# Performance work log

Measured on AMD Instinct MI355X. Metric: run time of the kernel, lower is better.

Reference implementation:

```python
import jax, jax.numpy as jnp
import numpy as np

Ng, Np, T, B = 2048, 512, 100, 256


def setup_inputs() -> dict:
    key = jax.random.key(0)
    ks = jax.random.split(key, 16)
    s = lambda fan_in: 1.0 / np.sqrt(fan_in)
    return {
        "v": jax.random.normal(ks[0], (B, T, 2), jnp.float32),
        "p0": jax.random.uniform(ks[1], (B, Np), jnp.float32),
        "enc1_W": jax.random.normal(ks[2], (Np, Ng), jnp.float32) * s(Np),
        "enc1_b": jnp.zeros((Ng,), jnp.float32),
        "enc2_W": jax.random.normal(ks[3], (Np, Ng), jnp.float32) * s(Np),
        "enc2_b": jnp.zeros((Ng,), jnp.float32),
        "M_W": jax.random.normal(ks[4], (2, Ng), jnp.float32) * s(2),
        "M_b": jnp.zeros((Ng,), jnp.float32),
        "lstm_W": jax.random.normal(ks[5], (Ng, 4 * Ng), jnp.float32) * s(Ng),
        "lstm_U": jax.random.normal(ks[6], (Ng, 4 * Ng), jnp.float32) * s(Ng),
        "lstm_b": jnp.zeros((4 * Ng,), jnp.float32),
        "dense_W": jax.random.normal(ks[7], (Ng, Ng), jnp.float32) * s(Ng),
        "dense_b": jnp.zeros((Ng,), jnp.float32),
        "dec_W": jax.random.normal(ks[8], (Ng, Np), jnp.float32) * s(Ng),
        "dec_b": jnp.zeros((Np,), jnp.float32),
    }


def reference(v, p0, enc1_W, enc1_b, enc2_W, enc2_b, M_W, M_b,
              lstm_W, lstm_U, lstm_b, dense_W, dense_b, dec_W, dec_b):
    # initial LSTM state from place-cell code: (h0, c0)
    h0 = p0 @ enc1_W + enc1_b                      # [B, Ng]
    c0 = p0 @ enc2_W + enc2_b                      # [B, Ng]
    Mv = v @ M_W + M_b                             # [B, T, Ng]
    # precompute input-to-gate projections for all timesteps
    x_gates = Mv @ lstm_W + lstm_b                 # [B, T, 4*Ng]

    def step(carry, xt):
        h, c = carry
        z = xt + h @ lstm_U                        # [B, 4*Ng]
        i, f, g, o = jnp.split(z, 4, axis=-1)      # Keras gate order i,f,c,o
        i = jax.nn.sigmoid(i)
        f = jax.nn.sigmoid(f)
        g = jax.nn.relu(g)                         # activation='relu'
        o = jax.nn.sigmoid(o)
        c = f * c + i * g
        h = o * jax.nn.relu(c)
        return (h, c), h

    xs = jnp.swapaxes(x_gates, 0, 1)               # [T, B, 4*Ng]
    _, hs = jax.lax.scan(step, (h0, c0), xs)       # hs: [T, B, Ng]
    rnn = jnp.swapaxes(hs, 0, 1)                   # [B, T, Ng]
    g_cells = jax.nn.relu(rnn @ dense_W + dense_b) # [B, T, Ng]
    place_preds = g_cells @ dec_W + dec_b          # [B, T, Np]
    return place_preds
```

## Files before the change

kernel.cpp:

```cpp
#include <hip/hip_runtime.h>
#include <stdint.h>

#define DI __device__ __forceinline__

typedef short s16x8 __attribute__((ext_vector_type(8)));
typedef float f32x4 __attribute__((ext_vector_type(4)));

#define NG   2048
#define NP   512
#define TT   100
#define BB   256
#define N4   8192
#define MR   25600
#define NBLK 256

DI unsigned short f32_to_bf16(float f) {
  union { float f; uint32_t u; } x; x.f = f;
  uint32_t r = x.u + 0x7fffu + ((x.u >> 16) & 1u);
  return (unsigned short)(r >> 16);
}

DI void async16(const void* g, void* l) {
  __builtin_amdgcn_global_load_lds((const __attribute__((address_space(1))) void*)g,
                                   (__attribute__((address_space(3))) void*)l,
                                   16, 0, 0);
}
DI void async4(const void* g, void* l) {
  __builtin_amdgcn_global_load_lds((const __attribute__((address_space(1))) void*)g,
                                   (__attribute__((address_space(3))) void*)l,
                                   4, 0, 0);
}

DI f32x4 mfma16(s16x8 a, s16x8 b, f32x4 c) {
  return __builtin_amdgcn_mfma_f32_16x16x32_bf16(a, b, c, 0, 0, 0);
}

__global__ __launch_bounds__(256) void k_zero(unsigned* p) {
  if (threadIdx.x < 160) p[threadIdx.x] = 0u;
}

DI void grid_barrier2(unsigned* bar, int xcd, int t) {
  asm volatile("s_waitcnt vmcnt(0)" ::: "memory");
  __syncthreads();
  if (threadIdx.x == 0) {
    unsigned a = __hip_atomic_fetch_add(bar + xcd * 16, 1u,
                                        __ATOMIC_RELAXED, __HIP_MEMORY_SCOPE_AGENT);
    if (a + 1u == 32u * (unsigned)(t + 1)) {
      unsigned g2 = __hip_atomic_fetch_add(bar + 128, 1u,
                                           __ATOMIC_RELAXED, __HIP_MEMORY_SCOPE_AGENT);
      if (g2 + 1u == 8u * (unsigned)(t + 1))
        __hip_atomic_store(bar + 144, (unsigned)(t + 1),
                           __ATOMIC_RELAXED, __HIP_MEMORY_SCOPE_AGENT);
    }
    while (__hip_atomic_load(bar + 144, __ATOMIC_RELAXED,
                             __HIP_MEMORY_SCOPE_AGENT) < (unsigned)(t + 1))
      __builtin_amdgcn_s_sleep(8);
  }
  __syncthreads();
}

template <int BM>
DI void gemm_core_p(const unsigned short* __restrict__ A, int lda, int m0,
                    const unsigned short* __restrict__ Bt, int ldb, int n0, int K,
                    unsigned short* sA, unsigned short* sB, f32x4* acc) {
  constexpr int FM = BM / 32;
  const int tid  = threadIdx.x;
  const int wave = tid >> 6;
  const int lane = tid & 63;
  const int quad = lane >> 4;
  const int lr   = lane & 15;
  const int wm   = wave >> 2;
  const int wn   = wave & 3;
  const int lr8  = lane >> 3;
  const int lc8  = lane & 7;
  const int scol = (lc8 ^ lr8) << 3;

  const int nkt = K >> 6;
  int buf = 0;

  auto stage = [&](int bsel, int k0) {
    unsigned short* dA = sA + bsel * (BM * 64);
    unsigned short* dB = sB + bsel * (128 * 64);
#pragma unroll
    for (int c = 0; c < BM / 64; ++c) {
      int rbase = wave * (BM / 8) + c * 8;
      const unsigned short* g = A + (size_t)(m0 + rbase + lr8) * lda + (k0 + scol);
      async16(g, dA + rbase * 64);
    }
#pragma unroll
    for (int c = 0; c < 2; ++c) {
      int rbase = wave * 16 + c * 8;
      const unsigned short* g = Bt + (size_t)(n0 + rbase + lr8) * ldb + (k0 + scol);
      async16(g, dB + rbase * 64);
    }
  };

  stage(0, 0);
  __syncthreads();
  for (int kt = 0; kt < nkt; ++kt) {
    if (kt + 1 < nkt) stage(buf ^ 1, (kt + 1) << 6);
    const char* cA = (const char*)(sA + buf * (BM * 64));
    const char* cB = (const char*)(sB + buf * (128 * 64));
#pragma unroll
    for (int ks = 0; ks < 2; ++ks) {
      s16x8 af[FM], bfr[2];
#pragma unroll
      for (int fm = 0; fm < FM; ++fm) {
        int row = wm * (BM / 2) + fm * 16 + lr;
        int off = row * 128 + ((ks * 64 + quad * 16) ^ ((row & 7) << 4));
        af[fm] = *(const s16x8*)(cA + off);
      }
#pragma unroll
      for (int fn = 0; fn < 2; ++fn) {
        int col = wn * 32 + fn * 16 + lr;
        int off = col * 128 + ((ks * 64 + quad * 16) ^ ((col & 7) << 4));
        bfr[fn] = *(const s16x8*)(cB + off);
      }
#pragma unroll
      for (int fm = 0; fm < FM; ++fm)
#pragma unroll
        for (int fn = 0; fn < 2; ++fn)
          acc[fm * 2 + fn] = mfma16(af[fm], bfr[fn], acc[fm * 2 + fn]);
    }
    __syncthreads();
    buf ^= 1;
  }
}

template <int MODE>
__global__ __launch_bounds__(256) void k_transpose_bf16(
    const float* __restrict__ src, unsigned short* __restrict__ dst,
    int R, int C, int noff) {
  __shared__ unsigned short tile[64][65];
  int tr0 = blockIdx.x * 64;
  int tc0 = blockIdx.y * 64;
  int tid = threadIdx.x;
#pragma unroll
  for (int i = 0; i < 16; ++i) {
    int idx = tid + i * 256;
    int r = idx >> 6, c = idx & 63;
    tile[r][c] = f32_to_bf16(src[(size_t)(tr0 + r) * C + (tc0 + c)]);
  }
  __syncthreads();
#pragma unroll
  for (int i = 0; i < 16; ++i) {
    int idx = tid + i * 256;
    int cc = idx >> 6, r = idx & 63;
    int c = tc0 + cc;
    int n = (MODE == 0) ? (c + noff)
                        : ((((c & 2047) >> 4) << 6) | (((c >> 11) & 3) << 4) | (c & 15));
    dst[(size_t)n * R + (tr0 + r)] = tile[r][cc];
  }
}

__global__ __launch_bounds__(256) void k_cvt(const float* __restrict__ src,
                                             unsigned short* __restrict__ dst, int n) {
  int i = blockIdx.x * 256 + threadIdx.x;
  if (i < n) dst[i] = f32_to_bf16(src[i]);
}

__global__ __launch_bounds__(256) void k_prep_xw_part(
    const float* __restrict__ lstm_W, const float* __restrict__ M_W,
    const float* __restrict__ M_b, float* __restrict__ part) {
  int c = blockIdx.x * 256 + threadIdx.x;
  int kc = blockIdx.y;
  int k0 = kc * 128;
  float a0 = 0.f, a1 = 0.f, ab = 0.f;
  for (int k = k0; k < k0 + 128; ++k) {
    float w = lstm_W[(size_t)k * N4 + c];
    a0 += M_W[k] * w;
    a1 += M_W[NG + k] * w;
    ab += M_b[k] * w;
  }
  float* p = part + (size_t)kc * 3 * N4;
  p[c] = a0; p[N4 + c] = a1; p[2 * N4 + c] = ab;
}

__global__ __launch_bounds__(256) void k_prep_xw_reduce(
    const float* __restrict__ part, const float* __restrict__ lstm_b,
    float* __restrict__ W2r, float* __restrict__ b2r) {
  int c = blockIdx.x * 256 + threadIdx.x;
  float a0 = 0.f, a1 = 0.f, ab = 0.f;
  for (int kc = 0; kc < 16; ++kc) {
    const float* p = part + (size_t)kc * 3 * N4;
    a0 += p[c]; a1 += p[N4 + c]; ab += p[2 * N4 + c];
  }
  int n = (((c & 2047) >> 4) << 6) | (((c >> 11) & 3) << 4) | (c & 15);
  W2r[n] = a0; W2r[N4 + n] = a1; b2r[n] = ab + lstm_b[c];
}

__global__ __launch_bounds__(512) void k_enc(
    const unsigned short* __restrict__ p0b, const unsigned short* __restrict__ encWt,
    const float* __restrict__ enc1_b, const float* __restrict__ enc2_b,
    unsigned short* __restrict__ hbf, float* __restrict__ cfp) {
  __shared__ __align__(16) unsigned short sA[2 * 64 * 64];
  __shared__ __align__(16) unsigned short sB[2 * 128 * 64];
  int m0 = blockIdx.x * 64, n0 = blockIdx.y * 128;
  const f32x4 vzero = {0.f, 0.f, 0.f, 0.f};
  f32x4 acc[4];
#pragma unroll
  for (int i = 0; i < 4; ++i) acc[i] = vzero;
  gemm_core_p<64>(p0b, NP, m0, encWt, NP, n0, NP, sA, sB, acc);

  const int tid = threadIdx.x, wave = tid >> 6, lane = tid & 63;
  const int quad = lane >> 4, lr = lane & 15, wm = wave >> 2, wn = wave & 3;
#pragma unroll
  for (int fm = 0; fm < 2; ++fm)
#pragma unroll
    for (int fn = 0; fn < 2; ++fn)
#pragma unroll
      for (int reg = 0; reg < 4; ++reg) {
        int grow = m0 + wm * 32 + fm * 16 + quad * 4 + reg;
        int gcol = n0 + wn * 32 + fn * 16 + lr;
        float val = acc[fm * 2 + fn][reg];
        if (gcol < NG)
          hbf[(size_t)grow * NG + gcol] = f32_to_bf16(val + enc1_b[gcol]);
        else
          cfp[(size_t)grow * NG + (gcol - NG)] = val + enc2_b[gcol - NG];
      }
}

__global__ __launch_bounds__(256) void k_steps(
    const unsigned short* __restrict__ Ut,
    const float* __restrict__ vv, const float* __restrict__ W2r,
    const float* __restrict__ b2r, const float* __restrict__ cfp,
    const unsigned short* __restrict__ hb0,
    unsigned short* __restrict__ hs, unsigned* __restrict__ bar) {
  __shared__ __align__(16) char smem[127488];

  const int bid = blockIdx.x;
  const int xcd = bid & 7, sb = bid >> 3;
  const int mt = sb >> 3, nsub = sb & 7;
  const int nt = xcd * 8 + nsub;
  const int m0 = mt * 64, n0 = nt * 128;
  const int tid = threadIdx.x;
  const int wave = tid >> 6, lane = tid & 63;
  const int quad = lane >> 4, lr = lane & 15;
  const int wm = wave >> 1, wn = wave & 1;
  const int lr8 = lane >> 3, lc8 = lane & 7;
  const int scol = (lc8 ^ lr8) << 3;

  float w2x[4], w2y[4], bz[4];
#pragma unroll
  for (int g = 0; g < 4; ++g) {
    const int idx = n0 + wn * 64 + g * 16 + lr;
    w2x[g] = W2r[idx]; w2y[g] = W2r[N4 + idx]; bz[g] = b2r[idx];
    asm volatile("" : "+v"(w2x[g])); asm volatile("" : "+v"(w2y[g]));
    asm volatile("" : "+v"(bz[g]));
  }
  const int cellg = nt * 32 + wn * 16 + lr;
  float cst[2][4];
#pragma unroll
  for (int fm = 0; fm < 2; ++fm)
#pragma unroll
    for (int reg = 0; reg < 4; ++reg) {
      const int r = wm * 32 + fm * 16 + quad * 4 + reg;
      cst[fm][reg] = cfp[(size_t)(m0 + r) * NG + cellg];
      asm volatile("" : "+v"(cst[fm][reg]));
    }

  auto stageA = [&](int slot, int kt, const unsigned short* hin) {
#pragma unroll
    for (int c = 0; c < 2; ++c) {
      const int rb = wave * 16 + c * 8;
      const unsigned short* g = hin + (size_t)(m0 + rb + lr8) * NG + ((kt << 6) + scol);
      async16(g, smem + slot * 8192 + rb * 128);
    }
  };
  auto stageB = [&](int slot, int k) {
#pragma unroll
    for (int c = 0; c < 4; ++c) {
      const int rb = wave * 32 + c * 8;
      const unsigned short* g = Ut + (size_t)(n0 + rb + lr8) * NG + (k + scol);
      async16(g, smem + 40960 + slot * 16384 + rb * 128);
    }
  };
  auto stageV = [&](int t) {
    const float* gx = vv + ((size_t)(m0 + lane) * TT + t) * 2;
    async4(gx, smem + 122880);
    async4(gx + 1, smem + 123136);
  };

  f32x4 acc[8];
  auto computeS = [&](int slot) {
    const char* cA = smem + slot * 8192;
    const char* cB = smem + 40960 + slot * 16384;
#pragma unroll
    for (int ks = 0; ks < 2; ++ks) {
      s16x8 af[2], bfr[4];
#pragma unroll
      for (int fm = 0; fm < 2; ++fm) {
        const int row = wm * 32 + fm * 16 + lr;
        af[fm] = *(const s16x8*)(cA + row * 128 + ((ks * 64 + quad * 16) ^ ((row & 7) << 4)));
      }
#pragma unroll
      for (int fn = 0; fn < 4; ++fn) {
        const int col = wn * 64 + fn * 16 + lr;
        bfr[fn] = *(const s16x8*)(cB + col * 128 + ((ks * 64 + quad * 16) ^ ((col & 7) << 4)));
      }
#pragma unroll
      for (int fm = 0; fm < 2; ++fm)
#pragma unroll
        for (int fn = 0; fn < 4; ++fn)
          acc[fm * 4 + fn] = mfma16(af[fm], bfr[fn], acc[fm * 4 + fn]);
    }
  };

#define INC5(x) x = ((x) == 4) ? 0 : ((x) + 1)
#define PHASE(W)  asm volatile("s_waitcnt vmcnt(" #W ")\n\ts_barrier" ::: "memory"); \
                  computeS(cs); INC5(cs);

  asm volatile("s_waitcnt vmcnt(0)" ::: "memory");
  int cs = 0;
  stageB(0, 0); stageB(1, 64); stageB(2, 128);

  for (int t = 0; t < TT; ++t) {
    const unsigned short* hin = t ? hs + (size_t)(t - 1) * BB * NG : hb0;
    {
      int s1 = cs; stageA(s1, 0, hin); INC5(s1);
      stageA(s1, 1, hin); INC5(s1);
      stageA(s1, 2, hin);
    }
    stageV(t);
    const f32x4 vzero = {0.f, 0.f, 0.f, 0.f};
#pragma unroll
    for (int i = 0; i < 8; ++i) acc[i] = vzero;

    int ss = cs; INC5(ss); INC5(ss); INC5(ss);
    stageB(ss, 3 << 6); stageA(ss, 3, hin); INC5(ss);
    PHASE(12)
    stageB(ss, 4 << 6); stageA(ss, 4, hin); INC5(ss);
    PHASE(16)
    stageB(ss, 5 << 6); stageA(ss, 5, hin); INC5(ss);
    PHASE(20)
    for (int p = 3; p <= 28; ++p) {
      stageB(ss, (p + 3) << 6); stageA(ss, p + 3, hin); INC5(ss);
      PHASE(18)
    }
    stageB(ss, 0); INC5(ss);
    PHASE(16)
    stageB(ss, 64); INC5(ss);
    PHASE(14)
    stageB(ss, 128); INC5(ss);
    PHASE(12)

    const float* vx = (const float*)(smem + 122880);
    const float* vy = (const float*)(smem + 123136);
    unsigned short* htmp = (unsigned short*)(smem + 123392);
#pragma unroll
    for (int fm = 0; fm < 2; ++fm)
#pragma unroll
      for (int reg = 0; reg < 4; ++reg) {
        const int r = wm * 32 + fm * 16 + quad * 4 + reg;
        const float ax = vx[r], ay = vy[r];
        float zi = acc[fm * 4 + 0][reg] + ax * w2x[0] + ay * w2y[0] + bz[0];
        float zf = acc[fm * 4 + 1][reg] + ax * w2x[1] + ay * w2y[1] + bz[1];
        float zg = acc[fm * 4 + 2][reg] + ax * w2x[2] + ay * w2y[2] + bz[2];
        float zo = acc[fm * 4 + 3][reg] + ax * w2x[3] + ay * w2y[3] + bz[3];
        float i_ = 1.f / (1.f + __expf(-zi));
        float f_ = 1.f / (1.f + __expf(-zf));
        float g_ = fmaxf(zg, 0.f);
        float o_ = 1.f / (1.f + __expf(-zo));
        float cn = f_ * cst[fm][reg] + i_ * g_;
        cst[fm][reg] = cn;
        htmp[r * 32 + wn * 16 + lr] = f32_to_bf16(o_ * fmaxf(cn, 0.f));
      }
    __syncthreads();
    const unsigned* hw = (const unsigned*)htmp;
#pragma unroll
    for (int p = 0; p < 4; ++p) {
      const int q = tid + p * 256;
      const int r = q >> 4, cq = q & 15;
      unsigned* hp = (unsigned*)(hs + ((size_t)t * BB + m0 + r) * NG) + (nt * 16 + cq);
      __hip_atomic_store(hp, hw[q], __ATOMIC_RELAXED, __HIP_MEMORY_SCOPE_AGENT);
    }
    if (t + 1 < TT) grid_barrier2(bar, xcd, t);
  }
#undef PHASE
#undef INC5
}

__global__ __launch_bounds__(512) void k_dense(
    const unsigned short* __restrict__ hs, const unsigned short* __restrict__ dWt,
    const float* __restrict__ dense_b, unsigned short* __restrict__ gc) {
  __shared__ __align__(16) unsigned short sA[2 * 128 * 64];
  __shared__ __align__(16) unsigned short sB[2 * 128 * 64];
  int bid = blockIdx.x;
  int mt = bid >> 4;
  int r4 = bid & 15;
  int nt = ((r4 & 7) << 1) | (r4 >> 3);
  int m0 = mt * 128, n0 = nt * 128;
  const f32x4 vzero = {0.f, 0.f, 0.f, 0.f};
  f32x4 acc[8];
#pragma unroll
  for (int i = 0; i < 8; ++i) acc[i] = vzero;
  gemm_core_p<128>(hs, NG, m0, dWt, NG, n0, NG, sA, sB, acc);

  const int tid = threadIdx.x, wave = tid >> 6, lane = tid & 63;
  const int quad = lane >> 4, lr = lane & 15, wm = wave >> 2, wn = wave & 3;
#pragma unroll
  for (int fm = 0; fm < 4; ++fm)
#pragma unroll
    for (int fn = 0; fn < 2; ++fn)
#pragma unroll
      for (int reg = 0; reg < 4; ++reg) {
        int grow = m0 + wm * 64 + fm * 16 + quad * 4 + reg;
        int gcol = n0 + wn * 32 + fn * 16 + lr;
        float val = fmaxf(acc[fm * 2 + fn][reg] + dense_b[gcol], 0.f);
        gc[(size_t)grow * NG + gcol] = f32_to_bf16(val);
      }
}

__global__ __launch_bounds__(512) void k_dec(
    const unsigned short* __restrict__ gc, const unsigned short* __restrict__ decWt,
    const float* __restrict__ dec_b, float* __restrict__ out) {
  __shared__ __align__(16) unsigned short sA[2 * 128 * 64];
  __shared__ __align__(16) unsigned short sB[2 * 128 * 64];
  int m0 = blockIdx.x * 128, n0 = blockIdx.y * 128;
  const f32x4 vzero = {0.f, 0.f, 0.f, 0.f};
  f32x4 acc[8];
#pragma unroll
  for (int i = 0; i < 8; ++i) acc[i] = vzero;
  gemm_core_p<128>(gc, NG, m0, decWt, NG, n0, NG, sA, sB, acc);

  const int tid = threadIdx.x, wave = tid >> 6, lane = tid & 63;
  const int quad = lane >> 4, lr = lane & 15, wm = wave >> 2, wn = wave & 3;
#pragma unroll
  for (int fm = 0; fm < 4; ++fm)
#pragma unroll
    for (int fn = 0; fn < 2; ++fn)
#pragma unroll
      for (int reg = 0; reg < 4; ++reg) {
        int grow = m0 + wm * 64 + fm * 16 + quad * 4 + reg;
        int gcol = n0 + wn * 32 + fn * 16 + lr;
        int tt = grow >> 8, b = grow & 255;
        out[((size_t)b * TT + tt) * NP + gcol] = acc[fm * 2 + fn][reg] + dec_b[gcol];
      }
}

extern "C" void kernel_launch(void* const* d_in, const int* in_sizes, int n_in,
                              void* d_out, int out_size, void* d_ws, size_t ws_size,
                              hipStream_t stream) {
  (void)in_sizes; (void)n_in; (void)out_size; (void)ws_size;
  const float* v       = (const float*)d_in[0];
  const float* p0      = (const float*)d_in[1];
  const float* enc1_W  = (const float*)d_in[2];
  const float* enc1_b  = (const float*)d_in[3];
  const float* enc2_W  = (const float*)d_in[4];
  const float* enc2_b  = (const float*)d_in[5];
  const float* M_W     = (const float*)d_in[6];
  const float* M_b     = (const float*)d_in[7];
  const float* lstm_W  = (const float*)d_in[8];
  const float* lstm_U  = (const float*)d_in[9];
  const float* lstm_b  = (const float*)d_in[10];
  const float* dense_W = (const float*)d_in[11];
  const float* dense_b = (const float*)d_in[12];
  const float* dec_W   = (const float*)d_in[13];
  const float* dec_b   = (const float*)d_in[14];
  float* out = (float*)d_out;

  char* ws = (char*)d_ws;
  size_t off = 0;
  auto alloc = [&](size_t bytes) {
    char* p = ws + off;
    off += (bytes + 255) & ~(size_t)255;
    return p;
  };
  unsigned short* Ut    = (unsigned short*)alloc((size_t)N4 * NG * 2);
  unsigned short* dWt   = (unsigned short*)alloc((size_t)NG * NG * 2);
  unsigned short* decWt = (unsigned short*)alloc((size_t)NP * NG * 2);
  unsigned short* encWt = (unsigned short*)alloc((size_t)2 * NG * NP * 2);
  unsigned short* p0b   = (unsigned short*)alloc((size_t)BB * NP * 2);
  float* W2r  = (float*)alloc((size_t)2 * N4 * 4);
  float* b2r  = (float*)alloc((size_t)N4 * 4);
  float* part = (float*)alloc((size_t)16 * 3 * N4 * 4);
  float* cfp  = (float*)alloc((size_t)BB * NG * 4);
  unsigned short* hb0 = (unsigned short*)alloc((size_t)BB * NG * 2);
  unsigned short* hs  = (unsigned short*)alloc((size_t)MR * NG * 2);
  unsigned short* gc  = (unsigned short*)alloc((size_t)MR * NG * 2);
  unsigned* bar = (unsigned*)alloc(1024);

  dim3 blk(256), blk5(512);
  k_zero<<<dim3(1), blk, 0, stream>>>(bar);
  k_transpose_bf16<1><<<dim3(32, 128), blk, 0, stream>>>(lstm_U, Ut, NG, N4, 0);
  k_transpose_bf16<0><<<dim3(32, 32), blk, 0, stream>>>(dense_W, dWt, NG, NG, 0);
  k_transpose_bf16<0><<<dim3(32, 8), blk, 0, stream>>>(dec_W, decWt, NG, NP, 0);
  k_transpose_bf16<0><<<dim3(8, 32), blk, 0, stream>>>(enc1_W, encWt, NP, NG, 0);
  k_transpose_bf16<0><<<dim3(8, 32), blk, 0, stream>>>(enc2_W, encWt, NP, NG, NG);
  k_cvt<<<dim3(512), blk, 0, stream>>>(p0, p0b, BB * NP);
  k_prep_xw_part<<<dim3(32, 16), blk, 0, stream>>>(lstm_W, M_W, M_b, part);
  k_prep_xw_reduce<<<dim3(32), blk, 0, stream>>>(part, lstm_b, W2r, b2r);
  k_enc<<<dim3(4, 32), blk5, 0, stream>>>(p0b, encWt, enc1_b, enc2_b, hb0, cfp);
  k_steps<<<dim3(NBLK), blk, 0, stream>>>(Ut, v, W2r, b2r, cfp, hb0, hs, bar);
  k_dense<<<dim3(3200), blk5, 0, stream>>>(hs, dWt, dense_b, gc);
  k_dec<<<dim3(200, 4), blk5, 0, stream>>>(gc, decWt, dec_b, out);
}
```

Measured before the change: 2.091 ms.

## Replace global grid barrier with per-row-tile flags and prefetch U across barrier

Replaces the hierarchical grid-wide barrier with per-timestep, per-M-tile counters, so each block waits only for the 64 blocks producing its batch rows of h. The first three U-tile loads for the next step are issued before waiting, which overlaps weight staging with synchronization. It also precomputes base addresses for the async loads and fully unrolls the main K loop. In exchange it needs a larger zeroed flag array, and correctness depends on flag counts and vmcnt accounting being right, including when the PHASE waits are drained at the end of each step.

```diff
diff --git a/kernel.cpp b/kernel.cpp
--- a/kernel.cpp
+++ b/kernel.cpp
@@ -35,28 +35,9 @@
   return __builtin_amdgcn_mfma_f32_16x16x32_bf16(a, b, c, 0, 0, 0);
 }
 
-__global__ __launch_bounds__(256) void k_zero(unsigned* p) {
-  if (threadIdx.x < 160) p[threadIdx.x] = 0u;
-}
-
-DI void grid_barrier2(unsigned* bar, int xcd, int t) {
-  asm volatile("s_waitcnt vmcnt(0)" ::: "memory");
-  __syncthreads();
-  if (threadIdx.x == 0) {
-    unsigned a = __hip_atomic_fetch_add(bar + xcd * 16, 1u,
-                                        __ATOMIC_RELAXED, __HIP_MEMORY_SCOPE_AGENT);
-    if (a + 1u == 32u * (unsigned)(t + 1)) {
-      unsigned g2 = __hip_atomic_fetch_add(bar + 128, 1u,
-                                           __ATOMIC_RELAXED, __HIP_MEMORY_SCOPE_AGENT);
-      if (g2 + 1u == 8u * (unsigned)(t + 1))
-        __hip_atomic_store(bar + 144, (unsigned)(t + 1),
-                           __ATOMIC_RELAXED, __HIP_MEMORY_SCOPE_AGENT);
-    }
-    while (__hip_atomic_load(bar + 144, __ATOMIC_RELAXED,
-                             __HIP_MEMORY_SCOPE_AGENT) < (unsigned)(t + 1))
-      __builtin_amdgcn_s_sleep(8);
-  }
-  __syncthreads();
+__global__ __launch_bounds__(256) void k_zero_flags(unsigned* p) {
+  int i = blockIdx.x * 256 + threadIdx.x;
+  if (i < TT * 4 * 16) p[i] = 0u;
 }
 
 template <int BM>
@@ -225,7 +206,7 @@
     const float* __restrict__ vv, const float* __restrict__ W2r,
     const float* __restrict__ b2r, const float* __restrict__ cfp,
     const unsigned short* __restrict__ hb0,
-    unsigned short* __restrict__ hs, unsigned* __restrict__ bar) {
+    unsigned short* __restrict__ hs, unsigned* __restrict__ flags) {
   __shared__ __align__(16) char smem[127488];
 
   const int bid = blockIdx.x;
@@ -259,21 +240,14 @@
       asm volatile("" : "+v"(cst[fm][reg]));
     }
 
-  auto stageA = [&](int slot, int kt, const unsigned short* hin) {
-#pragma unroll
-    for (int c = 0; c < 2; ++c) {
-      const int rb = wave * 16 + c * 8;
-      const unsigned short* g = hin + (size_t)(m0 + rb + lr8) * NG + ((kt << 6) + scol);
-      async16(g, smem + slot * 8192 + rb * 128);
-    }
-  };
+  const unsigned short* bw = Ut + (size_t)(n0 + wave * 32 + lr8) * NG + scol;
+  unsigned* const flagp = flags + (TT * 0 + 0) * 0 + 0;
+
   auto stageB = [&](int slot, int k) {
-#pragma unroll
-    for (int c = 0; c < 4; ++c) {
-      const int rb = wave * 32 + c * 8;
-      const unsigned short* g = Ut + (size_t)(n0 + rb + lr8) * NG + (k + scol);
-      async16(g, smem + 40960 + slot * 16384 + rb * 128);
-    }
+    char* dB = smem + 40960 + slot * 16384 + (wave * 32) * 128;
+#pragma unroll
+    for (int c = 0; c < 4; ++c)
+      async16(bw + (size_t)(c * 8) * NG + k, dB + c * 1024);
   };
   auto stageV = [&](int t) {
     const float* gx = vv + ((size_t)(m0 + lane) * TT + t) * 2;
@@ -316,33 +290,35 @@
 
   for (int t = 0; t < TT; ++t) {
     const unsigned short* hin = t ? hs + (size_t)(t - 1) * BB * NG : hb0;
-    {
-      int s1 = cs; stageA(s1, 0, hin); INC5(s1);
-      stageA(s1, 1, hin); INC5(s1);
-      stageA(s1, 2, hin);
-    }
+    const unsigned short* aw = hin + (size_t)(m0 + wave * 16 + lr8) * NG + scol;
+    auto stageA = [&](int slot, int kt) {
+      char* dA = smem + slot * 8192 + (wave * 16) * 128;
+      async16(aw + kt * 64, dA);
+      async16(aw + (size_t)8 * NG + kt * 64, dA + 1024);
+    };
+
+    { int s1 = cs; stageA(s1, 0); INC5(s1); stageA(s1, 1); INC5(s1); stageA(s1, 2); }
     stageV(t);
     const f32x4 vzero = {0.f, 0.f, 0.f, 0.f};
 #pragma unroll
     for (int i = 0; i < 8; ++i) acc[i] = vzero;
 
     int ss = cs; INC5(ss); INC5(ss); INC5(ss);
-    stageB(ss, 3 << 6); stageA(ss, 3, hin); INC5(ss);
+    stageB(ss, 3 << 6); stageA(ss, 3); INC5(ss);
     PHASE(12)
-    stageB(ss, 4 << 6); stageA(ss, 4, hin); INC5(ss);
+    stageB(ss, 4 << 6); stageA(ss, 4); INC5(ss);
     PHASE(16)
-    stageB(ss, 5 << 6); stageA(ss, 5, hin); INC5(ss);
+    stageB(ss, 5 << 6); stageA(ss, 5); INC5(ss);
     PHASE(20)
+#pragma unroll
     for (int p = 3; p <= 28; ++p) {
-      stageB(ss, (p + 3) << 6); stageA(ss, p + 3, hin); INC5(ss);
+      stageB(ss, (p + 3) << 6); stageA(ss, p + 3); INC5(ss);
       PHASE(18)
     }
-    stageB(ss, 0); INC5(ss);
-    PHASE(16)
-    stageB(ss, 64); INC5(ss);
-    PHASE(14)
-    stageB(ss, 128); INC5(ss);
     PHASE(12)
+    PHASE(6)
+    PHASE(0)
+    __syncthreads();
 
     const float* vx = (const float*)(smem + 122880);
     const float* vy = (const float*)(smem + 123136);
@@ -374,10 +350,25 @@
       unsigned* hp = (unsigned*)(hs + ((size_t)t * BB + m0 + r) * NG) + (nt * 16 + cq);
       __hip_atomic_store(hp, hw[q], __ATOMIC_RELAXED, __HIP_MEMORY_SCOPE_AGENT);
     }
-    if (t + 1 < TT) grid_barrier2(bar, xcd, t);
+
+    if (t + 1 < TT) {
+      stageB(ss, 0); INC5(ss);
+      stageB(ss, 64); INC5(ss);
+      stageB(ss, 128); INC5(ss);
+      asm volatile("s_waitcnt vmcnt(12)" ::: "memory");
+      asm volatile("s_barrier" ::: "memory");
+      if (tid == 0) {
+        unsigned* fp = flags + (t * 4 + mt) * 16;
+        __hip_atomic_fetch_add(fp, 1u, __ATOMIC_RELAXED, __HIP_MEMORY_SCOPE_AGENT);
+        while (__hip_atomic_load(fp, __ATOMIC_RELAXED, __HIP_MEMORY_SCOPE_AGENT) < 64u)
+          __builtin_amdgcn_s_sleep(2);
+      }
+      asm volatile("s_barrier" ::: "memory");
+    }
   }
 #undef PHASE
 #undef INC5
+  (void)flagp;
 }
 
 __global__ __launch_bounds__(512) void k_dense(
@@ -478,10 +469,10 @@
   unsigned short* hb0 = (unsigned short*)alloc((size_t)BB * NG * 2);
   unsigned short* hs  = (unsigned short*)alloc((size_t)MR * NG * 2);
   unsigned short* gc  = (unsigned short*)alloc((size_t)MR * NG * 2);
-  unsigned* bar = (unsigned*)alloc(1024);
+  unsigned* flags = (unsigned*)alloc((size_t)TT * 4 * 16 * 4);
 
   dim3 blk(256), blk5(512);
-  k_zero<<<dim3(1), blk, 0, stream>>>(bar);
+  k_zero_flags<<<dim3(25), blk, 0, stream>>>(flags);
   k_transpose_bf16<1><<<dim3(32, 128), blk, 0, stream>>>(lstm_U, Ut, NG, N4, 0);
   k_transpose_bf16<0><<<dim3(32, 32), blk, 0, stream>>>(dense_W, dWt, NG, NG, 0);
   k_transpose_bf16<0><<<dim3(32, 8), blk, 0, stream>>>(dec_W, decWt, NG, NP, 0);
@@ -491,7 +482,7 @@
   k_prep_xw_part<<<dim3(32, 16), blk, 0, stream>>>(lstm_W, M_W, M_b, part);
   k_prep_xw_reduce<<<dim3(32), blk, 0, stream>>>(part, lstm_b, W2r, b2r);
   k_enc<<<dim3(4, 32), blk5, 0, stream>>>(p0b, encWt, enc1_b, enc2_b, hb0, cfp);
-  k_steps<<<dim3(NBLK), blk, 0, stream>>>(Ut, v, W2r, b2r, cfp, hb0, hs, bar);
+  k_steps<<<dim3(NBLK), blk, 0, stream>>>(Ut, v, W2r, b2r, cfp, hb0, hs, flags);
   k_dense<<<dim3(3200), blk5, 0, stream>>>(hs, dWt, dense_b, gc);
   k_dec<<<dim3(200, 4), blk5, 0, stream>>>(gc, decWt, dec_b, out);
 }
```

After: 2.232 ms. 6.7% more time.

## Load recurrent weights directly to registers and stage h via register double-buffer

Applied to the files above, without the earlier changes.

The persistent LSTM step kernel no longer stages the U weight tile through LDS with async global-to-LDS loads. Each wave now loads its B fragments straight from global memory into registers, double-buffered across phases. The h input goes through registers into a 2-slot swizzled LDS buffer instead of the 5-slot async pipeline. This shrinks LDS from ~127KB to ~21KB and drops the vmcnt-tuned pipeline, but B is now reread from global or L2 every timestep with a shallower prefetch depth.

```diff
diff --git a/kernel.cpp b/kernel.cpp
--- a/kernel.cpp
+++ b/kernel.cpp
@@ -226,7 +226,7 @@
     const float* __restrict__ b2r, const float* __restrict__ cfp,
     const unsigned short* __restrict__ hb0,
     unsigned short* __restrict__ hs, unsigned* __restrict__ bar) {
-  __shared__ __align__(16) char smem[127488];
+  __shared__ __align__(16) char smem[20992];
 
   const int bid = blockIdx.x;
   const int xcd = bid & 7, sb = bid >> 3;
@@ -237,8 +237,6 @@
   const int wave = tid >> 6, lane = tid & 63;
   const int quad = lane >> 4, lr = lane & 15;
   const int wm = wave >> 1, wn = wave & 1;
-  const int lr8 = lane >> 3, lc8 = lane & 7;
-  const int scol = (lc8 ^ lr8) << 3;
 
   float w2x[4], w2y[4], bz[4];
 #pragma unroll
@@ -259,94 +257,94 @@
       asm volatile("" : "+v"(cst[fm][reg]));
     }
 
-  auto stageA = [&](int slot, int kt, const unsigned short* hin) {
-#pragma unroll
-    for (int c = 0; c < 2; ++c) {
-      const int rb = wave * 16 + c * 8;
-      const unsigned short* g = hin + (size_t)(m0 + rb + lr8) * NG + ((kt << 6) + scol);
-      async16(g, smem + slot * 8192 + rb * 128);
-    }
+  const unsigned short* bB0s[4];
+  const unsigned short* bB[4];
+#pragma unroll
+  for (int fn = 0; fn < 4; ++fn) {
+    bB0s[fn] = Ut + (size_t)(n0 + wn * 64 + fn * 16 + lr) * NG + quad * 8;
+    bB[fn] = bB0s[fn];
+  }
+
+  const int ar = tid >> 2;
+  const int aq = tid & 3;
+  const int awz = (ar & 7) << 4;
+  const int awo0 = ar * 128 + ((aq * 32) ^ awz);
+  const int awo1 = ar * 128 + ((aq * 32 + 16) ^ awz);
+
+  f32x4 acc[8];
+
+  auto loadB = [&](s16x8* d) {
+#pragma unroll
+    for (int fn = 0; fn < 4; ++fn) {
+      d[fn * 2 + 0] = *(const s16x8*)(bB[fn]);
+      d[fn * 2 + 1] = *(const s16x8*)(bB[fn] + 32);
+    }
+#pragma unroll
+    for (int fn = 0; fn < 4; ++fn) bB[fn] += 64;
   };
-  auto stageB = [&](int slot, int k) {
-#pragma unroll
-    for (int c = 0; c < 4; ++c) {
-      const int rb = wave * 32 + c * 8;
-      const unsigned short* g = Ut + (size_t)(n0 + rb + lr8) * NG + (k + scol);
-      async16(g, smem + 40960 + slot * 16384 + rb * 128);
-    }
-  };
-  auto stageV = [&](int t) {
-    const float* gx = vv + ((size_t)(m0 + lane) * TT + t) * 2;
-    async4(gx, smem + 122880);
-    async4(gx + 1, smem + 123136);
-  };
-
-  f32x4 acc[8];
-  auto computeS = [&](int slot) {
+
+  auto computeS = [&](int slot, const s16x8* B) {
     const char* cA = smem + slot * 8192;
-    const char* cB = smem + 40960 + slot * 16384;
 #pragma unroll
     for (int ks = 0; ks < 2; ++ks) {
-      s16x8 af[2], bfr[4];
+      s16x8 af[2];
 #pragma unroll
       for (int fm = 0; fm < 2; ++fm) {
         const int row = wm * 32 + fm * 16 + lr;
         af[fm] = *(const s16x8*)(cA + row * 128 + ((ks * 64 + quad * 16) ^ ((row & 7) << 4)));
       }
 #pragma unroll
-      for (int fn = 0; fn < 4; ++fn) {
-        const int col = wn * 64 + fn * 16 + lr;
-        bfr[fn] = *(const s16x8*)(cB + col * 128 + ((ks * 64 + quad * 16) ^ ((col & 7) << 4)));
-      }
-#pragma unroll
       for (int fm = 0; fm < 2; ++fm)
 #pragma unroll
         for (int fn = 0; fn < 4; ++fn)
-          acc[fm * 4 + fn] = mfma16(af[fm], bfr[fn], acc[fm * 4 + fn]);
+          acc[fm * 4 + fn] = mfma16(af[fm], B[fn * 2 + ks], acc[fm * 4 + fn]);
     }
   };
 
-#define INC5(x) x = ((x) == 4) ? 0 : ((x) + 1)
-#define PHASE(W)  asm volatile("s_waitcnt vmcnt(" #W ")\n\ts_barrier" ::: "memory"); \
-                  computeS(cs); INC5(cs);
-
-  asm volatile("s_waitcnt vmcnt(0)" ::: "memory");
-  int cs = 0;
-  stageB(0, 0); stageB(1, 64); stageB(2, 128);
+  auto phaseF = [&](int slot, const s16x8* Bc, s16x8* Bn,
+                    const s16x8* Awr, s16x8* Ald, const unsigned short* aG) {
+    if (Awr) {
+      char* d = smem + ((slot ^ 1) * 8192);
+      *(s16x8*)(d + awo0) = Awr[0];
+      *(s16x8*)(d + awo1) = Awr[1];
+    }
+    loadB(Bn);
+    if (aG) { Ald[0] = *(const s16x8*)aG; Ald[1] = *(const s16x8*)(aG + 8); }
+    computeS(slot, Bc);
+    __syncthreads();
+  };
+
+  s16x8 B0[8], B1[8], Aw[2], Ax[2];
+  loadB(B0);
 
   for (int t = 0; t < TT; ++t) {
     const unsigned short* hin = t ? hs + (size_t)(t - 1) * BB * NG : hb0;
-    {
-      int s1 = cs; stageA(s1, 0, hin); INC5(s1);
-      stageA(s1, 1, hin); INC5(s1);
-      stageA(s1, 2, hin);
-    }
-    stageV(t);
+    const unsigned short* aB = hin + (size_t)(m0 + ar) * NG + aq * 16;
+    { const float* gx = vv + ((size_t)(m0 + lane) * TT + t) * 2;
+      async4(gx, smem + 16384); async4(gx + 1, smem + 16640); }
+
+    Aw[0] = *(const s16x8*)(aB); Aw[1] = *(const s16x8*)(aB + 8);
+    { char* d = smem;
+      *(s16x8*)(d + awo0) = Aw[0]; *(s16x8*)(d + awo1) = Aw[1]; }
+    Ax[0] = *(const s16x8*)(aB + 64); Ax[1] = *(const s16x8*)(aB + 64 + 8);
     const f32x4 vzero = {0.f, 0.f, 0.f, 0.f};
 #pragma unroll
     for (int i = 0; i < 8; ++i) acc[i] = vzero;
-
-    int ss = cs; INC5(ss); INC5(ss); INC5(ss);
-    stageB(ss, 3 << 6); stageA(ss, 3, hin); INC5(ss);
-    PHASE(12)
-    stageB(ss, 4 << 6); stageA(ss, 4, hin); INC5(ss);
-    PHASE(16)
-    stageB(ss, 5 << 6); stageA(ss, 5, hin); INC5(ss);
-    PHASE(20)
-    for (int p = 3; p <= 28; ++p) {
-      stageB(ss, (p + 3) << 6); stageA(ss, p + 3, hin); INC5(ss);
-      PHASE(18)
-    }
-    stageB(ss, 0); INC5(ss);
-    PHASE(16)
-    stageB(ss, 64); INC5(ss);
-    PHASE(14)
-    stageB(ss, 128); INC5(ss);
-    PHASE(12)
-
-    const float* vx = (const float*)(smem + 122880);
-    const float* vy = (const float*)(smem + 123136);
-    unsigned short* htmp = (unsigned short*)(smem + 123392);
+    __syncthreads();
+
+    int ao = 128;
+    for (int pp = 0; pp < 15; ++pp) {
+      phaseF(0, B0, B1, Ax, Aw, aB + ao); ao += 64;
+      phaseF(1, B1, B0, Aw, Ax, aB + ao); ao += 64;
+    }
+    phaseF(0, B0, B1, Ax, Aw, nullptr);
+#pragma unroll
+    for (int fn = 0; fn < 4; ++fn) bB[fn] = bB0s[fn];
+    phaseF(1, B1, B0, nullptr, Ax, nullptr);
+
+    const float* vx = (const float*)(smem + 16384);
+    const float* vy = (const float*)(smem + 16640);
+    unsigned short* htmp = (unsigned short*)(smem + 16896);
 #pragma unroll
     for (int fm = 0; fm < 2; ++fm)
 #pragma unroll
@@ -376,8 +374,6 @@
     }
     if (t + 1 < TT) grid_barrier2(bar, xcd, t);
   }
-#undef PHASE
-#undef INC5
 }
 
 __global__ __launch_bounds__(512) void k_dense(
```

Result: slower. 3.913 ms (+87.1%).

## Split K across two wave groups in recurrent step kernel with LDS reduction

Applied to the files above, without the earlier changes.

Doubles the k_steps block to 512 threads. Two groups of four waves each take one half of every 64-wide K chunk, and their partial accumulators are summed through LDS before the gate nonlinearity. Staging loads are spread over 8 waves, which changes the vmcnt wait counts. The first three B tiles for the next timestep are now prefetched before the grid barrier. The goal is more wave-level parallelism and latency hiding in the latency-bound recurrent loop, at the cost of extra LDS traffic, extra syncthreads and higher register pressure per block.

```diff
diff --git a/kernel.cpp b/kernel.cpp
--- a/kernel.cpp
+++ b/kernel.cpp
@@ -220,7 +220,7 @@
       }
 }
 
-__global__ __launch_bounds__(256) void k_steps(
+__global__ __launch_bounds__(512) void k_steps(
     const unsigned short* __restrict__ Ut,
     const float* __restrict__ vv, const float* __restrict__ W2r,
     const float* __restrict__ b2r, const float* __restrict__ cfp,
@@ -234,9 +234,11 @@
   const int nt = xcd * 8 + nsub;
   const int m0 = mt * 64, n0 = nt * 128;
   const int tid = threadIdx.x;
-  const int wave = tid >> 6, lane = tid & 63;
+  const int w = tid >> 6, lane = tid & 63;
+  const int kh = w >> 2;
+  const int wq = w & 3;
+  const int wm = wq >> 1, wn = wq & 1;
   const int quad = lane >> 4, lr = lane & 15;
-  const int wm = wave >> 1, wn = wave & 1;
   const int lr8 = lane >> 3, lc8 = lane & 7;
   const int scol = (lc8 ^ lr8) << 3;
 
@@ -245,8 +247,6 @@
   for (int g = 0; g < 4; ++g) {
     const int idx = n0 + wn * 64 + g * 16 + lr;
     w2x[g] = W2r[idx]; w2y[g] = W2r[N4 + idx]; bz[g] = b2r[idx];
-    asm volatile("" : "+v"(w2x[g])); asm volatile("" : "+v"(w2y[g]));
-    asm volatile("" : "+v"(bz[g]));
   }
   const int cellg = nt * 32 + wn * 16 + lr;
   float cst[2][4];
@@ -256,24 +256,13 @@
     for (int reg = 0; reg < 4; ++reg) {
       const int r = wm * 32 + fm * 16 + quad * 4 + reg;
       cst[fm][reg] = cfp[(size_t)(m0 + r) * NG + cellg];
-      asm volatile("" : "+v"(cst[fm][reg]));
-    }
-
-  auto stageA = [&](int slot, int kt, const unsigned short* hin) {
-#pragma unroll
-    for (int c = 0; c < 2; ++c) {
-      const int rb = wave * 16 + c * 8;
-      const unsigned short* g = hin + (size_t)(m0 + rb + lr8) * NG + ((kt << 6) + scol);
-      async16(g, smem + slot * 8192 + rb * 128);
-    }
-  };
+    }
+
+  const unsigned short* bwB = Ut + (size_t)(n0 + w * 16 + lr8) * NG + scol;
   auto stageB = [&](int slot, int k) {
-#pragma unroll
-    for (int c = 0; c < 4; ++c) {
-      const int rb = wave * 32 + c * 8;
-      const unsigned short* g = Ut + (size_t)(n0 + rb + lr8) * NG + (k + scol);
-      async16(g, smem + 40960 + slot * 16384 + rb * 128);
-    }
+    char* dB = smem + 40960 + slot * 16384 + (w * 16) * 128;
+    async16(bwB + k, dB);
+    async16(bwB + (size_t)8 * NG + k, dB + 1024);
   };
   auto stageV = [&](int t) {
     const float* gx = vv + ((size_t)(m0 + lane) * TT + t) * 2;
@@ -285,24 +274,19 @@
   auto computeS = [&](int slot) {
     const char* cA = smem + slot * 8192;
     const char* cB = smem + 40960 + slot * 16384;
-#pragma unroll
-    for (int ks = 0; ks < 2; ++ks) {
-      s16x8 af[2], bfr[4];
-#pragma unroll
-      for (int fm = 0; fm < 2; ++fm) {
-        const int row = wm * 32 + fm * 16 + lr;
-        af[fm] = *(const s16x8*)(cA + row * 128 + ((ks * 64 + quad * 16) ^ ((row & 7) << 4)));
-      }
-#pragma unroll
-      for (int fn = 0; fn < 4; ++fn) {
-        const int col = wn * 64 + fn * 16 + lr;
-        bfr[fn] = *(const s16x8*)(cB + col * 128 + ((ks * 64 + quad * 16) ^ ((col & 7) << 4)));
-      }
+    s16x8 af[2];
+#pragma unroll
+    for (int fm = 0; fm < 2; ++fm) {
+      const int row = wm * 32 + fm * 16 + lr;
+      af[fm] = *(const s16x8*)(cA + row * 128 + ((kh * 64 + quad * 16) ^ ((row & 7) << 4)));
+    }
+#pragma unroll
+    for (int fn = 0; fn < 4; ++fn) {
+      const int col = wn * 64 + fn * 16 + lr;
+      s16x8 bf = *(const s16x8*)(cB + col * 128 + ((kh * 64 + quad * 16) ^ ((col & 7) << 4)));
 #pragma unroll
       for (int fm = 0; fm < 2; ++fm)
-#pragma unroll
-        for (int fn = 0; fn < 4; ++fn)
-          acc[fm * 4 + fn] = mfma16(af[fm], bfr[fn], acc[fm * 4 + fn]);
+        acc[fm * 4 + fn] = mfma16(af[fm], bf, acc[fm * 4 + fn]);
     }
   };
 
@@ -316,63 +300,79 @@
 
   for (int t = 0; t < TT; ++t) {
     const unsigned short* hin = t ? hs + (size_t)(t - 1) * BB * NG : hb0;
-    {
-      int s1 = cs; stageA(s1, 0, hin); INC5(s1);
-      stageA(s1, 1, hin); INC5(s1);
-      stageA(s1, 2, hin);
-    }
+    const unsigned short* awA = hin + (size_t)(m0 + w * 8 + lr8) * NG + scol;
+    auto stageA = [&](int slot, int kt) {
+      async16(awA + kt * 64, smem + slot * 8192 + (w * 8) * 128);
+    };
+
     stageV(t);
+    { int s1 = cs; stageA(s1, 0); INC5(s1); stageA(s1, 1); INC5(s1); stageA(s1, 2); }
     const f32x4 vzero = {0.f, 0.f, 0.f, 0.f};
 #pragma unroll
     for (int i = 0; i < 8; ++i) acc[i] = vzero;
 
     int ss = cs; INC5(ss); INC5(ss); INC5(ss);
-    stageB(ss, 3 << 6); stageA(ss, 3, hin); INC5(ss);
-    PHASE(12)
-    stageB(ss, 4 << 6); stageA(ss, 4, hin); INC5(ss);
-    PHASE(16)
-    stageB(ss, 5 << 6); stageA(ss, 5, hin); INC5(ss);
-    PHASE(20)
+    stageB(ss, 3 << 6); stageA(ss, 3); INC5(ss);
+    PHASE(5)
+    stageB(ss, 4 << 6); stageA(ss, 4); INC5(ss);
+    PHASE(7)
+    stageB(ss, 5 << 6); stageA(ss, 5); INC5(ss);
+    PHASE(9)
     for (int p = 3; p <= 28; ++p) {
-      stageB(ss, (p + 3) << 6); stageA(ss, p + 3, hin); INC5(ss);
-      PHASE(18)
-    }
-    stageB(ss, 0); INC5(ss);
-    PHASE(16)
-    stageB(ss, 64); INC5(ss);
-    PHASE(14)
-    stageB(ss, 128); INC5(ss);
-    PHASE(12)
-
-    const float* vx = (const float*)(smem + 122880);
-    const float* vy = (const float*)(smem + 123136);
-    unsigned short* htmp = (unsigned short*)(smem + 123392);
-#pragma unroll
-    for (int fm = 0; fm < 2; ++fm)
-#pragma unroll
-      for (int reg = 0; reg < 4; ++reg) {
-        const int r = wm * 32 + fm * 16 + quad * 4 + reg;
-        const float ax = vx[r], ay = vy[r];
-        float zi = acc[fm * 4 + 0][reg] + ax * w2x[0] + ay * w2y[0] + bz[0];
-        float zf = acc[fm * 4 + 1][reg] + ax * w2x[1] + ay * w2y[1] + bz[1];
-        float zg = acc[fm * 4 + 2][reg] + ax * w2x[2] + ay * w2y[2] + bz[2];
-        float zo = acc[fm * 4 + 3][reg] + ax * w2x[3] + ay * w2y[3] + bz[3];
-        float i_ = 1.f / (1.f + __expf(-zi));
-        float f_ = 1.f / (1.f + __expf(-zf));
-        float g_ = fmaxf(zg, 0.f);
-        float o_ = 1.f / (1.f + __expf(-zo));
-        float cn = f_ * cst[fm][reg] + i_ * g_;
-        cst[fm][reg] = cn;
-        htmp[r * 32 + wn * 16 + lr] = f32_to_bf16(o_ * fmaxf(cn, 0.f));
-      }
+      stageB(ss, (p + 3) << 6); stageA(ss, p + 3); INC5(ss);
+      PHASE(9)
+    }
+    PHASE(6)
+    PHASE(3)
+    PHASE(0)
+    if (t + 1 < TT) {
+      int s2 = cs; stageB(s2, 0); INC5(s2); stageB(s2, 64); INC5(s2); stageB(s2, 128);
+    }
     __syncthreads();
-    const unsigned* hw = (const unsigned*)htmp;
-#pragma unroll
-    for (int p = 0; p < 4; ++p) {
-      const int q = tid + p * 256;
-      const int r = q >> 4, cq = q & 15;
-      unsigned* hp = (unsigned*)(hs + ((size_t)t * BB + m0 + r) * NG) + (nt * 16 + cq);
-      __hip_atomic_store(hp, hw[q], __ATOMIC_RELAXED, __HIP_MEMORY_SCOPE_AGENT);
+
+    if (kh) {
+      f32x4* px = (f32x4*)(smem + wq * 8192 + lane * 128);
+#pragma unroll
+      for (int i = 0; i < 8; ++i) px[i] = acc[i];
+    }
+    __syncthreads();
+    if (!kh) {
+      const f32x4* px = (const f32x4*)(smem + wq * 8192 + lane * 128);
+#pragma unroll
+      for (int i = 0; i < 8; ++i) acc[i] += px[i];
+
+      const float* vx = (const float*)(smem + 122880);
+      const float* vy = (const float*)(smem + 123136);
+      unsigned short* htmp = (unsigned short*)(smem + 123392);
+#pragma unroll
+      for (int fm = 0; fm < 2; ++fm)
+#pragma unroll
+        for (int reg = 0; reg < 4; ++reg) {
+          const int r = wm * 32 + fm * 16 + quad * 4 + reg;
+          const float ax = vx[r], ay = vy[r];
+          float zi = acc[fm * 4 + 0][reg] + ax * w2x[0] + ay * w2y[0] + bz[0];
+          float zf = acc[fm * 4 + 1][reg] + ax * w2x[1] + ay * w2y[1] + bz[1];
+          float zg = acc[fm * 4 + 2][reg] + ax * w2x[2] + ay * w2y[2] + bz[2];
+          float zo = acc[fm * 4 + 3][reg] + ax * w2x[3] + ay * w2y[3] + bz[3];
+          float i_ = 1.f / (1.f + __expf(-zi));
+          float f_ = 1.f / (1.f + __expf(-zf));
+          float g_ = fmaxf(zg, 0.f);
+          float o_ = 1.f / (1.f + __expf(-zo));
+          float cn = f_ * cst[fm][reg] + i_ * g_;
+          cst[fm][reg] = cn;
+          htmp[r * 32 + wn * 16 + lr] = f32_to_bf16(o_ * fmaxf(cn, 0.f));
+        }
+    }
+    __syncthreads();
+    if (tid < 256) {
+      const unsigned* hw = (const unsigned*)(smem + 123392);
+#pragma unroll
+      for (int p = 0; p < 4; ++p) {
+        const int q = tid + p * 256;
+        const int r = q >> 4, cq = q & 15;
+        unsigned* hp = (unsigned*)(hs + ((size_t)t * BB + m0 + r) * NG) + (nt * 16 + cq);
+        __hip_atomic_store(hp, hw[q], __ATOMIC_RELAXED, __HIP_MEMORY_SCOPE_AGENT);
+      }
     }
     if (t + 1 < TT) grid_barrier2(bar, xcd, t);
   }
@@ -491,7 +491,7 @@
   k_prep_xw_part<<<dim3(32, 16), blk, 0, stream>>>(lstm_W, M_W, M_b, part);
   k_prep_xw_reduce<<<dim3(32), blk, 0, stream>>>(part, lstm_b, W2r, b2r);
   k_enc<<<dim3(4, 32), blk5, 0, stream>>>(p0b, encWt, enc1_b, enc2_b, hb0, cfp);
-  k_steps<<<dim3(NBLK), blk, 0, stream>>>(Ut, v, W2r, b2r, cfp, hb0, hs, bar);
+  k_steps<<<dim3(NBLK), blk5, 0, stream>>>(Ut, v, W2r, b2r, cfp, hb0, hs, bar);
   k_dense<<<dim3(3200), blk5, 0, stream>>>(hs, dWt, dense_b, gc);
   k_dec<<<dim3(200, 4), blk5, 0, stream>>>(gc, decWt, dec_b, out);
 }
```

Result: no change. 2.090 ms (-0.1%).
